# Performance work log

Measured on AMD Instinct MI355X. Metric: run time of the kernel, lower is better.

## Reference

```python
import jax, jax.numpy as jnp
import numpy as np

FILTER_WEIGHTS = [1, 2, 1]
B, C, H, W = 8, 128, 256, 256


def _create_lowpass_kernel(weights):
    k1 = np.convolve(weights, [1, 1]).reshape(1, -1)  # [1,3,3,1]
    k = k1.T @ k1                                     # 4x4 binomial kernel
    return (k / k.sum()).astype(np.float32)


def setup_inputs() -> dict:
    key = jax.random.key(0)
    x = jax.random.normal(key, (B, C, H, W), dtype=jnp.float32)
    kernel = jnp.asarray(_create_lowpass_kernel(FILTER_WEIGHTS))  # (4,4)
    return {"x": x, "kernel": kernel}


def reference(x, kernel):
    # Depthwise blur + stride-2 downsample, padding = len(filter_weights)//2 = 1.
    b, c, h, w = x.shape
    kh, kw = kernel.shape
    radius = len(FILTER_WEIGHTS) // 2
    # depthwise kernel: (C, 1, kh, kw), same kernel for every channel
    k = jnp.broadcast_to(kernel.astype(x.dtype)[None, None], (c, 1, kh, kw))
    y = jax.lax.conv_general_dilated(
        x, k,
        window_strides=(2, 2),
        padding=[(radius, radius), (radius, radius)],
        dimension_numbers=("NCHW", "OIHW", "NCHW"),
        feature_group_count=c,
    )
    return y  # (B, C, H//2, W//2)
```

## Files before the change

kernel.cpp:

```cpp
#include <hip/hip_runtime.h>
#include <hip/hip_bf16.h>


#define IN_H 256
#define IN_W 256
#define OUT_H 128
#define OUT_W 128

__device__ __forceinline__ void hrow(const float* __restrict__ xp, int r,
                                     int lane, float& h0, float& h1) {
    const int rc  = min(max(r, 0), IN_H - 1);
    const float m = (r == rc) ? 1.0f : 0.0f;
    const float4 v = *(const float4*)(xp + (size_t)rc * IN_W + 4 * lane);
    float prev = __shfl_up(v.w, 1);
    float next = __shfl_down(v.x, 1);
    prev = (lane == 0)  ? 0.0f : prev;
    next = (lane == 63) ? 0.0f : next;
    h0 = m * (prev + 3.0f * v.x + 3.0f * v.y + v.z);
    h1 = m * (v.y + 3.0f * v.z + 3.0f * v.w + next);
}

__device__ __forceinline__ void nt_store2(float* p, float a, float b) {
    float2 o; o.x = a; o.y = b;
    __builtin_nontemporal_store(*(double*)&o, (double*)p);
}

__global__ __launch_bounds__(256, 8) void downsample_kernel(
    const float* __restrict__ x, float* __restrict__ y) {
    const int plane = blockIdx.y;
    const int q     = blockIdx.x * 4 + (threadIdx.x >> 6);
    const int lane  = threadIdx.x & 63;
    const float* __restrict__ xp = x + (size_t)plane * IN_H * IN_W;
    float* __restrict__ yp =
        y + (size_t)plane * OUT_H * OUT_W + (size_t)(4 * q) * OUT_W;
    const float s = 1.0f / 64.0f;

    float h[6][2];
    #pragma unroll
    for (int k = 0; k < 6; ++k)
        hrow(xp, 8 * q - 1 + k, lane, h[k][0], h[k][1]);

    nt_store2(yp + 2 * lane,
              (h[0][0] + 3.0f * h[1][0] + 3.0f * h[2][0] + h[3][0]) * s,
              (h[0][1] + 3.0f * h[1][1] + 3.0f * h[2][1] + h[3][1]) * s);
    nt_store2(yp + OUT_W + 2 * lane,
              (h[2][0] + 3.0f * h[3][0] + 3.0f * h[4][0] + h[5][0]) * s,
              (h[2][1] + 3.0f * h[3][1] + 3.0f * h[4][1] + h[5][1]) * s);

    float g[4][2];
    #pragma unroll
    for (int k = 0; k < 4; ++k)
        hrow(xp, 8 * q + 5 + k, lane, g[k][0], g[k][1]);

    nt_store2(yp + 2 * OUT_W + 2 * lane,
              (h[4][0] + 3.0f * h[5][0] + 3.0f * g[0][0] + g[1][0]) * s,
              (h[4][1] + 3.0f * h[5][1] + 3.0f * g[0][1] + g[1][1]) * s);
    nt_store2(yp + 3 * OUT_W + 2 * lane,
              (g[0][0] + 3.0f * g[1][0] + 3.0f * g[2][0] + g[3][0]) * s,
              (g[0][1] + 3.0f * g[1][1] + 3.0f * g[2][1] + g[3][1]) * s);
}

extern "C" void kernel_launch(void* const* d_in, const int* in_sizes, int n_in,
                              void* d_out, int out_size, void* d_ws, size_t ws_size,
                              hipStream_t stream) {
    (void)n_in; (void)d_ws; (void)ws_size; (void)out_size;
    const float* x = (const float*)d_in[0];
    float* y = (float*)d_out;
    const int planes = in_sizes[0] / (IN_H * IN_W);
    dim3 grid(8, planes);
    dim3 block(256);
    downsample_kernel<<<grid, block, 0, stream>>>(x, y);
}
```

Measured before the change: 53.69 us.

## Process 16 output rows per wave with a rolling horizontal-row window

Each wavefront now produces 16 output rows instead of 4, looping over 8 steps. It carries the last two horizontally filtered rows across steps, so halo rows are loaded once per 16 outputs instead of once per 4. The grid shrinks from 8 to 2 blocks per plane, cutting redundant halo loads and block count. In exchange there are fewer waves in flight (2048 blocks), which could reduce latency hiding on a memory-bound kernel.

Result: slower. 56.80 us (+5.8%).

```diff
diff --git a/kernel.cpp b/kernel.cpp
--- a/kernel.cpp
+++ b/kernel.cpp
@@ -28,36 +28,34 @@
 __global__ __launch_bounds__(256, 8) void downsample_kernel(
     const float* __restrict__ x, float* __restrict__ y) {
     const int plane = blockIdx.y;
-    const int q     = blockIdx.x * 4 + (threadIdx.x >> 6);
+    const int s     = blockIdx.x * 4 + (threadIdx.x >> 6);
     const int lane  = threadIdx.x & 63;
     const float* __restrict__ xp = x + (size_t)plane * IN_H * IN_W;
     float* __restrict__ yp =
-        y + (size_t)plane * OUT_H * OUT_W + (size_t)(4 * q) * OUT_W;
-    const float s = 1.0f / 64.0f;
+        y + (size_t)plane * OUT_H * OUT_W + (size_t)(16 * s) * OUT_W;
+    const int rbase = 32 * s;
+    const float sc = 1.0f / 64.0f;
 
-    float h[6][2];
+    float c[2][2], g[4][2];
+    hrow(xp, rbase - 1, lane, c[0][0], c[0][1]);
+    hrow(xp, rbase,     lane, c[1][0], c[1][1]);
+
     #pragma unroll
-    for (int k = 0; k < 6; ++k)
-        hrow(xp, 8 * q - 1 + k, lane, h[k][0], h[k][1]);
+    for (int t = 0; t < 8; ++t) {
+        #pragma unroll
+        for (int k = 0; k < 4; ++k)
+            hrow(xp, rbase + 4 * t + 1 + k, lane, g[k][0], g[k][1]);
 
-    nt_store2(yp + 2 * lane,
-              (h[0][0] + 3.0f * h[1][0] + 3.0f * h[2][0] + h[3][0]) * s,
-              (h[0][1] + 3.0f * h[1][1] + 3.0f * h[2][1] + h[3][1]) * s);
-    nt_store2(yp + OUT_W + 2 * lane,
-              (h[2][0] + 3.0f * h[3][0] + 3.0f * h[4][0] + h[5][0]) * s,
-              (h[2][1] + 3.0f * h[3][1] + 3.0f * h[4][1] + h[5][1]) * s);
+        nt_store2(yp + (size_t)(2 * t) * OUT_W + 2 * lane,
+                  (c[0][0] + 3.0f * c[1][0] + 3.0f * g[0][0] + g[1][0]) * sc,
+                  (c[0][1] + 3.0f * c[1][1] + 3.0f * g[0][1] + g[1][1]) * sc);
+        nt_store2(yp + (size_t)(2 * t + 1) * OUT_W + 2 * lane,
+                  (g[0][0] + 3.0f * g[1][0] + 3.0f * g[2][0] + g[3][0]) * sc,
+                  (g[0][1] + 3.0f * g[1][1] + 3.0f * g[2][1] + g[3][1]) * sc);
 
-    float g[4][2];
-    #pragma unroll
-    for (int k = 0; k < 4; ++k)
-        hrow(xp, 8 * q + 5 + k, lane, g[k][0], g[k][1]);
-
-    nt_store2(yp + 2 * OUT_W + 2 * lane,
-              (h[4][0] + 3.0f * h[5][0] + 3.0f * g[0][0] + g[1][0]) * s,
-              (h[4][1] + 3.0f * h[5][1] + 3.0f * g[0][1] + g[1][1]) * s);
-    nt_store2(yp + 3 * OUT_W + 2 * lane,
-              (g[0][0] + 3.0f * g[1][0] + 3.0f * g[2][0] + g[3][0]) * s,
-              (g[0][1] + 3.0f * g[1][1] + 3.0f * g[2][1] + g[3][1]) * s);
+        c[0][0] = g[2][0]; c[0][1] = g[2][1];
+        c[1][0] = g[3][0]; c[1][1] = g[3][1];
+    }
 }
 
 extern "C" void kernel_launch(void* const* d_in, const int* in_sizes, int n_in,
@@ -67,7 +65,7 @@
     const float* x = (const float*)d_in[0];
     float* y = (float*)d_out;
     const int planes = in_sizes[0] / (IN_H * IN_W);
-    dim3 grid(8, planes);
+    dim3 grid(2, planes);
     dim3 block(256);
     downsample_kernel<<<grid, block, 0, stream>>>(x, y);
 }
```
